# Kernel optimization log

Hardware: AMD Instinct MI355X
Metric: run time of the kernel (lower is better)

Reference implementation:

```python
import jax, jax.numpy as jnp
import numpy as np

NUM_HEADS = 16


def setup_inputs() -> dict:
    key = jax.random.key(0)
    k1, k2, k3 = jax.random.split(key, 3)
    B, S, E = 2, 2048, 1024
    hidden_states = jax.random.normal(k1, (B, S, E), dtype=jnp.float32)
    c_attn_w = jax.random.normal(k2, (E, 3 * E), dtype=jnp.float32) * 0.02
    c_attn_b = jnp.zeros((3 * E,), dtype=jnp.float32)
    c_proj_w = jax.random.normal(k3, (E, E), dtype=jnp.float32) * 0.02
    c_proj_b = jnp.zeros((E,), dtype=jnp.float32)
    return {
        "hidden_states": hidden_states,
        "c_attn_w": c_attn_w,
        "c_attn_b": c_attn_b,
        "c_proj_w": c_proj_w,
        "c_proj_b": c_proj_b,
    }


def reference(hidden_states, c_attn_w, c_attn_b, c_proj_w, c_proj_b):
    B, S, E = hidden_states.shape
    H = NUM_HEADS
    D = E // H
    # Conv1D: qkv projection -> [B, S, 3E]
    qkv = jnp.einsum("bse,ef->bsf", hidden_states, c_attn_w) + c_attn_b
    q, k, v = jnp.split(qkv, 3, axis=-1)
    # split heads -> [B, H, S, D]
    def heads(x):
        return x.reshape(B, S, H, D).transpose(0, 2, 1, 3)
    q, k, v = heads(q), heads(k), heads(v)
    # scaled QK^T -> [B, H, S, S]
    scale = jnp.asarray(D, dtype=q.dtype) ** 0.5
    attn_weights = jnp.einsum("bhqd,bhkd->bhqk", q, k) / scale
    # causal mask (bias buffer): True on/below diagonal
    causal = jnp.tril(jnp.ones((S, S), dtype=bool))
    mask_value = jnp.finfo(attn_weights.dtype).min
    attn_weights = jnp.where(causal[None, None, :, :], attn_weights, mask_value)
    attn_weights = jax.nn.softmax(attn_weights, axis=-1)
    # attn @ V -> merge heads -> [B, S, E]
    attn_out = jnp.einsum("bhqk,bhkd->bhqd", attn_weights, v)
    attn_out = attn_out.transpose(0, 2, 1, 3).reshape(B, S, E)
    # output projection (Conv1D)
    out = jnp.einsum("bse,ef->bsf", attn_out, c_proj_w) + c_proj_b
    return out
```

## Files before the change

kernel.cpp:

```cpp
#include <hip/hip_runtime.h>
#include <stdint.h>

typedef __attribute__((ext_vector_type(8))) __bf16 bf16x8;
typedef __attribute__((ext_vector_type(4))) __bf16 bf16x4;
typedef __attribute__((ext_vector_type(4))) float f32x4;

#define MFMA16(a, b, c) __builtin_amdgcn_mfma_f32_16x16x32_bf16(a, b, c, 0, 0, 0)

__device__ __forceinline__ void async_ld16(const __bf16* g, __bf16* lds_base) {
    __builtin_amdgcn_global_load_lds(
        (const __attribute__((address_space(1))) void*)g,
        (__attribute__((address_space(3))) void*)lds_base, 16, 0, 0);
}

__global__ __launch_bounds__(256) void k_prep(
    const float* __restrict__ hs, const float* __restrict__ w1,
    const float* __restrict__ w2, __bf16* __restrict__ hsb,
    __bf16* __restrict__ w1t, __bf16* __restrict__ w2t) {
    __shared__ __bf16 tile[32][33];
    int bid = blockIdx.x, tid = threadIdx.x;
    if (bid < 4096) {
        int i = (bid * 256 + tid) * 4;
        float4 v = *(const float4*)(hs + i);
        bf16x4 o;
        o.x = (__bf16)v.x; o.y = (__bf16)v.y; o.z = (__bf16)v.z; o.w = (__bf16)v.w;
        *(bf16x4*)(hsb + i) = o;
        return;
    }
    const float* in; __bf16* out; int C, tb;
    if (bid < 7168) { in = w1; out = w1t; C = 3072; tb = bid - 4096; }
    else            { in = w2; out = w2t; C = 1024; tb = bid - 7168; }
    const int R = 1024;
    int ntc = C >> 5;
    int c0 = (tb % ntc) * 32, r0 = (tb / ntc) * 32;
    int tx = tid & 31, ty = tid >> 5;
#pragma unroll
    for (int i = 0; i < 4; i++)
        tile[ty + i * 8][tx] = (__bf16)in[(size_t)(r0 + ty + i * 8) * C + c0 + tx];
    __syncthreads();
#pragma unroll
    for (int i = 0; i < 4; i++)
        out[(size_t)(c0 + ty + i * 8) * R + r0 + tx] = tile[tx][ty + i * 8];
}

__global__ __launch_bounds__(256, 3) void k_gemm_qkv(
    const __bf16* __restrict__ A, const __bf16* __restrict__ Bt,
    const float* __restrict__ bias,
    __bf16* __restrict__ Qo, __bf16* __restrict__ Ko, __bf16* __restrict__ Vo) {
    __shared__ __bf16 As[128 * 32];
    __shared__ __bf16 Bs[128 * 32];
    const int Kd = 1024;
    int lid = blockIdx.x;
    int xcd = lid & 7, c = lid >> 3;
    int mi = (xcd >> 1) * 8 + c / 12;
    int ni = (xcd & 1) * 12 + c % 12;
    int n0 = ni * 128, m0 = mi * 128;
    bool tr = (ni < 16);
    int tid = threadIdx.x;
    int wv = tid >> 6, lane = tid & 63;
    int wm = (wv >> 1) * 64, wn = (wv & 1) * 64;
    int quad = lane >> 4, l16 = lane & 15;
    int lrow = lane >> 2, lcol = (lane & 3) * 8;
    const __bf16* p0 = tr ? Bs : As;
    const __bf16* p1 = tr ? As : Bs;
    int o0 = tr ? wn : wm, o1 = tr ? wm : wn;
    f32x4 acc[4][4] = {};
    for (int k0 = 0; k0 < Kd; k0 += 32) {
        __syncthreads();
#pragma unroll
        for (int r = 0; r < 2; r++) {
            int row = r * 64 + wv * 16;
            async_ld16(&A[(size_t)(m0 + row + lrow) * Kd + k0 + lcol], &As[row * 32]);
            async_ld16(&Bt[(size_t)(n0 + row + lrow) * Kd + k0 + lcol], &Bs[row * 32]);
        }
        __syncthreads();
        bf16x8 f0[4], f1[4];
#pragma unroll
        for (int i = 0; i < 4; i++)
            f0[i] = *(const bf16x8*)(&p0[(o0 + i * 16 + l16) * 32 + quad * 8]);
#pragma unroll
        for (int j = 0; j < 4; j++)
            f1[j] = *(const bf16x8*)(&p1[(o1 + j * 16 + l16) * 32 + quad * 8]);
#pragma unroll
        for (int i = 0; i < 4; i++)
#pragma unroll
            for (int j = 0; j < 4; j++)
                acc[i][j] = MFMA16(f0[i], f1[j], acc[i][j]);
    }
    if (tr) {
#pragma unroll
        for (int i = 0; i < 4; i++) {
#pragma unroll
            for (int j = 0; j < 4; j++) {
                int nb = n0 + wn + i * 16 + quad * 4;
                int sec = nb >> 10, nl = nb & 1023;
                int h = nl >> 6, d = nl & 63;
                int sg = m0 + wm + j * 16 + l16;
                int bb = sg >> 11, s = sg & 2047;
                f32x4 bv = *(const f32x4*)(&bias[nb]);
                __bf16* dst = (sec == 0) ? Qo : Ko;
                float scl = (sec == 0) ? 0.1803368801f : 1.0f;
                bf16x4 q4;
#pragma unroll
                for (int r = 0; r < 4; r++)
                    q4[r] = (__bf16)((acc[i][j][r] + bv[r]) * scl);
                *(bf16x4*)(&dst[((size_t)(bb * 16 + h) * 2048 + s) * 64 + d]) = q4;
            }
        }
    } else {
#pragma unroll
        for (int i = 0; i < 4; i++) {
#pragma unroll
            for (int j = 0; j < 4; j++) {
                int n = n0 + wn + j * 16 + l16;
                float bv = bias[n];
                int nl = n & 1023;
                int h = nl >> 6, d = nl & 63;
                int mbase = m0 + wm + i * 16 + quad * 4;
                int bb = mbase >> 11, s = mbase & 2047;
                bf16x4 v4;
#pragma unroll
                for (int r = 0; r < 4; r++) v4[r] = (__bf16)(acc[i][j][r] + bv);
                *(bf16x4*)(&Vo[((size_t)(bb * 16 + h) * 64 + d) * 2048 + s]) = v4;
            }
        }
    }
}

__global__ __launch_bounds__(256, 3) void k_gemm_proj(
    const __bf16* __restrict__ A, const __bf16* __restrict__ Bt,
    const float* __restrict__ bias, float* __restrict__ out) {
    __shared__ __bf16 As[64 * 32];
    __shared__ __bf16 Bs[128 * 32];
    const int Kd = 1024;
    int lid = blockIdx.x;
    int xcd = lid & 7, c = lid >> 3;
    int mi = xcd * 8 + (c >> 3);
    int ni = c & 7;
    int n0 = ni * 128, m0 = mi * 64;
    int tid = threadIdx.x;
    int wv = tid >> 6, lane = tid & 63;
    int wm = (wv >> 1) * 32, wn = (wv & 1) * 64;
    int quad = lane >> 4, l16 = lane & 15;
    int lrow = lane >> 2, lcol = (lane & 3) * 8;
    f32x4 acc[4][2] = {};
    for (int k0 = 0; k0 < Kd; k0 += 32) {
        __syncthreads();
        async_ld16(&A[(size_t)(m0 + wv * 16 + lrow) * Kd + k0 + lcol], &As[(wv * 16) * 32]);
#pragma unroll
        for (int r = 0; r < 2; r++) {
            int row = r * 64 + wv * 16;
            async_ld16(&Bt[(size_t)(n0 + row + lrow) * Kd + k0 + lcol], &Bs[row * 32]);
        }
        __syncthreads();
        bf16x8 f0[4], f1[2];
#pragma unroll
        for (int i = 0; i < 4; i++)
            f0[i] = *(const bf16x8*)(&Bs[(wn + i * 16 + l16) * 32 + quad * 8]);
#pragma unroll
        for (int j = 0; j < 2; j++)
            f1[j] = *(const bf16x8*)(&As[(wm + j * 16 + l16) * 32 + quad * 8]);
#pragma unroll
        for (int i = 0; i < 4; i++)
#pragma unroll
            for (int j = 0; j < 2; j++)
                acc[i][j] = MFMA16(f0[i], f1[j], acc[i][j]);
    }
#pragma unroll
    for (int i = 0; i < 4; i++) {
#pragma unroll
        for (int j = 0; j < 2; j++) {
            int nb = n0 + wn + i * 16 + quad * 4;
            int m = m0 + wm + j * 16 + l16;
            f32x4 bv = *(const f32x4*)(&bias[nb]);
            f32x4 o = acc[i][j] + bv;
            *(f32x4*)(&out[(size_t)m * 1024 + nb]) = o;
        }
    }
}

__device__ const int ATT_ORDER[24] = {7, 8, 10, 12, 14, 16, 18, 20, 22, 23, 6, 21,
                                      5, 19, 4, 17, 3, 15, 2, 13, 1, 11, 0, 9};

__global__ __launch_bounds__(256, 3) void k_attn(
    const __bf16* __restrict__ Qg, const __bf16* __restrict__ Kg,
    const __bf16* __restrict__ Vtg, __bf16* __restrict__ Op, float* __restrict__ Lp) {
    __shared__ __bf16 Ksb[2][64 * 64];
    __shared__ __bf16 Vtb[2][64 * 64];
    __shared__ __bf16 Ps[128 * 72];
    int bh = blockIdx.x & 31;
    int slot = ATT_ORDER[blockIdx.x >> 5];
    int t, k0, k1;
    if (slot < 8) { t = slot; k0 = 0; k1 = 2 * t + 2; }
    else { int i2 = slot - 8; t = 8 + (i2 >> 1); k0 = (i2 & 1) * 16; k1 = min(k0 + 16, 2 * t + 2); }
    const __bf16* Qp = Qg + (size_t)bh * 2048 * 64;
    const __bf16* Kp = Kg + (size_t)bh * 2048 * 64;
    const __bf16* Vp = Vtg + (size_t)bh * 64 * 2048;
    int tid = threadIdx.x, wv = tid >> 6, lane = tid & 63;
    int quad = lane >> 4, l16 = lane & 15;
    int rl = lane >> 3, sj = lane & 7;
    int sgo = (sj ^ rl) << 3;
    int swl = l16 & 7;

    bf16x8 qf[2][2];
#pragma unroll
    for (int qn = 0; qn < 2; qn++)
#pragma unroll
        for (int ks = 0; ks < 2; ks++)
            qf[qn][ks] = *(const bf16x8*)(
                &Qp[(size_t)(t * 128 + wv * 32 + qn * 16 + l16) * 64 + ks * 32 + quad * 8]);
    const f32x4 zf = {0.f, 0.f, 0.f, 0.f};
    f32x4 lacc[2] = {zf, zf};
    f32x4 acc_o[2][4] = {};

    auto stage = [&](int buf, int kt) {
#pragma unroll
        for (int half = 0; half < 2; half++) {
            int r0 = wv * 16 + half * 8;
            async_ld16(&Kp[(size_t)(kt * 64 + r0 + rl) * 64 + sgo], &Ksb[buf][r0 * 64]);
            async_ld16(&Vp[(size_t)(r0 + rl) * 2048 + kt * 64 + sgo], &Vtb[buf][r0 * 64]);
        }
    };

    stage(0, k0);
    __syncthreads();

    for (int kt = k0; kt < k1; kt++) {
        int cur = (kt - k0) & 1;
        if (kt + 1 < k1) stage(cur ^ 1, kt + 1);
        const __bf16* Kc = Ksb[cur];
        const __bf16* Vc = Vtb[cur];
        f32x4 s[2][4];
#pragma unroll
        for (int ks = 0; ks < 2; ks++) {
            bf16x8 kf[4];
#pragma unroll
            for (int i = 0; i < 4; i++)
                kf[i] = *(const bf16x8*)(
                    &Kc[(i * 16 + l16) * 64 + (((ks * 4 + quad) ^ swl) << 3)]);
            __builtin_amdgcn_s_setprio(1);
#pragma unroll
            for (int i = 0; i < 4; i++)
#pragma unroll
                for (int qn = 0; qn < 2; qn++)
                    s[qn][i] = MFMA16(kf[i], qf[qn][ks], ks == 0 ? zf : s[qn][i]);
            __builtin_amdgcn_s_setprio(0);
        }
#pragma unroll
        for (int qn = 0; qn < 2; qn++) {
            int qmin = t * 128 + wv * 32 + qn * 16;
            if (kt * 64 + 63 > qmin) {
#pragma unroll
                for (int i = 0; i < 4; i++)
#pragma unroll
                    for (int r = 0; r < 4; r++)
                        if (kt * 64 + i * 16 + quad * 4 + r > qmin + l16) s[qn][i][r] = -1e30f;
            }
        }
#pragma unroll
        for (int qn = 0; qn < 2; qn++)
#pragma unroll
            for (int i = 0; i < 4; i++) {
                f32x4 pe;
#pragma unroll
                for (int r = 0; r < 4; r++) pe[r] = exp2f(s[qn][i][r]);
                lacc[qn] += pe;
                bf16x4 pk;
#pragma unroll
                for (int r = 0; r < 4; r++) pk[r] = (__bf16)pe[r];
                *(bf16x4*)(&Ps[(wv * 32 + qn * 16 + l16) * 72 + i * 16 + quad * 4]) = pk;
            }
#pragma unroll
        for (int ks = 0; ks < 2; ks++) {
            bf16x8 pf[2];
#pragma unroll
            for (int qn = 0; qn < 2; qn++)
                pf[qn] = *(const bf16x8*)(
                    &Ps[(wv * 32 + qn * 16 + l16) * 72 + ks * 32 + quad * 8]);
            bf16x8 vf[4];
#pragma unroll
            for (int i = 0; i < 4; i++)
                vf[i] = *(const bf16x8*)(
                    &Vc[(i * 16 + l16) * 64 + (((ks * 4 + quad) ^ swl) << 3)]);
            __builtin_amdgcn_s_setprio(1);
#pragma unroll
            for (int i = 0; i < 4; i++)
#pragma unroll
                for (int qn = 0; qn < 2; qn++)
                    acc_o[qn][i] = MFMA16(vf[i], pf[qn], acc_o[qn][i]);
            __builtin_amdgcn_s_setprio(0);
        }
        __syncthreads();
    }
    size_t pbase = (size_t)slot * 32 + bh;
#pragma unroll
    for (int qn = 0; qn < 2; qn++) {
        float ls = lacc[qn][0] + lacc[qn][1] + lacc[qn][2] + lacc[qn][3];
        ls += __shfl_xor(ls, 16);
        ls += __shfl_xor(ls, 32);
        int ql = wv * 32 + qn * 16 + l16;
        if (quad == 0) Lp[pbase * 128 + ql] = ls;
#pragma unroll
        for (int i = 0; i < 4; i++) {
            bf16x4 o4;
#pragma unroll
            for (int r = 0; r < 4; r++) o4[r] = (__bf16)acc_o[qn][i][r];
            *(bf16x4*)(&Op[(pbase * 128 + ql) * 64 + i * 16 + quad * 4]) = o4;
        }
    }
}

__global__ __launch_bounds__(256) void k_attn_combine(
    const __bf16* __restrict__ Op, const float* __restrict__ Lp,
    __bf16* __restrict__ AOb) {
    int gid = blockIdx.x * 256 + threadIdx.x;
    int d4 = gid & 15;
    int q = (gid >> 4) & 2047;
    int bh = gid >> 15;
    int t = q >> 7, ql = q & 127;
    int n = (t <= 7) ? 1 : 2;
    int base = (t <= 7) ? t : 8 + 2 * (t - 8);
    float L = 0.f, o[4] = {};
    for (int c = 0; c < n; c++) {
        size_t idx = (size_t)(base + c) * 32 + bh;
        L += Lp[idx * 128 + ql];
        bf16x4 p4 = *(const bf16x4*)(&Op[(idx * 128 + ql) * 64 + d4 * 4]);
#pragma unroll
        for (int r = 0; r < 4; r++) o[r] += (float)p4[r];
    }
    float inv = 1.f / L;
    int b = bh >> 4, h = bh & 15;
    bf16x4 o4;
#pragma unroll
    for (int r = 0; r < 4; r++) o4[r] = (__bf16)(o[r] * inv);
    *(bf16x4*)(&AOb[((size_t)b * 2048 + q) * 1024 + h * 64 + d4 * 4]) = o4;
}

extern "C" void kernel_launch(void* const* d_in, const int* in_sizes, int n_in,
                              void* d_out, int out_size, void* d_ws, size_t ws_size,
                              hipStream_t stream) {
    const float* hs = (const float*)d_in[0];
    const float* w1 = (const float*)d_in[1];
    const float* b1 = (const float*)d_in[2];
    const float* w2 = (const float*)d_in[3];
    const float* b2 = (const float*)d_in[4];
    float* out = (float*)d_out;

    char* ws = (char*)d_ws;
    __bf16* hsb = (__bf16*)(ws);
    __bf16* w1t = (__bf16*)(ws + (size_t)8 * 1024 * 1024);
    __bf16* w2t = (__bf16*)(ws + (size_t)14 * 1024 * 1024);
    __bf16* Qb  = (__bf16*)(ws + (size_t)16 * 1024 * 1024);
    __bf16* Kb  = (__bf16*)(ws + (size_t)24 * 1024 * 1024);
    __bf16* Vb  = (__bf16*)(ws + (size_t)32 * 1024 * 1024);
    __bf16* AOb = (__bf16*)(ws + (size_t)40 * 1024 * 1024);
    __bf16* Opart = (__bf16*)(ws);
    float*  Lpart = (float*)(ws + (size_t)13 * 1024 * 1024);

    k_prep<<<8192, 256, 0, stream>>>(hs, w1, w2, hsb, w1t, w2t);
    k_gemm_qkv<<<768, 256, 0, stream>>>(hsb, w1t, b1, Qb, Kb, Vb);
    k_attn<<<768, 256, 0, stream>>>(Qb, Kb, Vb, Opart, Lpart);
    k_attn_combine<<<4096, 256, 0, stream>>>(Opart, Lpart, AOb);
    k_gemm_proj<<<512, 256, 0, stream>>>(AOb, w2t, b2, out);
}
```

Before: 183.2 us.

## Double GEMM K-tile to 64 with swizzled LDS, skip masked attention tiles, reorder blocks

Both GEMM kernels now stage 64-wide K slices with an XOR-swizzled LDS layout, which halves the number of barrier pairs per K loop and is meant to cut LDS bank conflicts. The attention kernel lets each wave skip the compute for key tiles that lie entirely above its causal rows, while still taking part in staging and barriers. The attention block launch order table is also reshuffled to rebalance the work. The larger LDS footprint in the GEMMs may lower occupancy.

```diff
diff --git a/kernel.cpp b/kernel.cpp
--- a/kernel.cpp
+++ b/kernel.cpp
@@ -47,8 +47,8 @@
     const __bf16* __restrict__ A, const __bf16* __restrict__ Bt,
     const float* __restrict__ bias,
     __bf16* __restrict__ Qo, __bf16* __restrict__ Ko, __bf16* __restrict__ Vo) {
-    __shared__ __bf16 As[128 * 32];
-    __shared__ __bf16 Bs[128 * 32];
+    __shared__ __bf16 As[128 * 64];
+    __shared__ __bf16 Bs[128 * 64];
     const int Kd = 1024;
     int lid = blockIdx.x;
     int xcd = lid & 7, c = lid >> 3;
@@ -60,32 +60,39 @@
     int wv = tid >> 6, lane = tid & 63;
     int wm = (wv >> 1) * 64, wn = (wv & 1) * 64;
     int quad = lane >> 4, l16 = lane & 15;
-    int lrow = lane >> 2, lcol = (lane & 3) * 8;
+    int rl = lane >> 3, sj = lane & 7;
+    int sgo = (sj ^ rl) << 3;
+    int swl = l16 & 7;
     const __bf16* p0 = tr ? Bs : As;
     const __bf16* p1 = tr ? As : Bs;
     int o0 = tr ? wn : wm, o1 = tr ? wm : wn;
     f32x4 acc[4][4] = {};
-    for (int k0 = 0; k0 < Kd; k0 += 32) {
-        __syncthreads();
-#pragma unroll
-        for (int r = 0; r < 2; r++) {
-            int row = r * 64 + wv * 16;
-            async_ld16(&A[(size_t)(m0 + row + lrow) * Kd + k0 + lcol], &As[row * 32]);
-            async_ld16(&Bt[(size_t)(n0 + row + lrow) * Kd + k0 + lcol], &Bs[row * 32]);
-        }
-        __syncthreads();
-        bf16x8 f0[4], f1[4];
-#pragma unroll
-        for (int i = 0; i < 4; i++)
-            f0[i] = *(const bf16x8*)(&p0[(o0 + i * 16 + l16) * 32 + quad * 8]);
-#pragma unroll
-        for (int j = 0; j < 4; j++)
-            f1[j] = *(const bf16x8*)(&p1[(o1 + j * 16 + l16) * 32 + quad * 8]);
-#pragma unroll
-        for (int i = 0; i < 4; i++)
+    for (int k0 = 0; k0 < Kd; k0 += 64) {
+        __syncthreads();
+#pragma unroll
+        for (int r = 0; r < 4; r++) {
+            int row = wv * 32 + r * 8;
+            async_ld16(&A[(size_t)(m0 + row + rl) * Kd + k0 + sgo], &As[row * 64]);
+            async_ld16(&Bt[(size_t)(n0 + row + rl) * Kd + k0 + sgo], &Bs[row * 64]);
+        }
+        __syncthreads();
+#pragma unroll
+        for (int ks = 0; ks < 2; ks++) {
+            bf16x8 f0[4], f1[4];
+#pragma unroll
+            for (int i = 0; i < 4; i++)
+                f0[i] = *(const bf16x8*)(
+                    &p0[(o0 + i * 16 + l16) * 64 + (((ks * 4 + quad) ^ swl) << 3)]);
 #pragma unroll
             for (int j = 0; j < 4; j++)
-                acc[i][j] = MFMA16(f0[i], f1[j], acc[i][j]);
+                f1[j] = *(const bf16x8*)(
+                    &p1[(o1 + j * 16 + l16) * 64 + (((ks * 4 + quad) ^ swl) << 3)]);
+#pragma unroll
+            for (int i = 0; i < 4; i++)
+#pragma unroll
+                for (int j = 0; j < 4; j++)
+                    acc[i][j] = MFMA16(f0[i], f1[j], acc[i][j]);
+        }
     }
     if (tr) {
 #pragma unroll
@@ -130,8 +137,8 @@
 __global__ __launch_bounds__(256, 3) void k_gemm_proj(
     const __bf16* __restrict__ A, const __bf16* __restrict__ Bt,
     const float* __restrict__ bias, float* __restrict__ out) {
-    __shared__ __bf16 As[64 * 32];
-    __shared__ __bf16 Bs[128 * 32];
+    __shared__ __bf16 As[64 * 64];
+    __shared__ __bf16 Bs[128 * 64];
     const int Kd = 1024;
     int lid = blockIdx.x;
     int xcd = lid & 7, c = lid >> 3;
@@ -142,29 +149,40 @@
     int wv = tid >> 6, lane = tid & 63;
     int wm = (wv >> 1) * 32, wn = (wv & 1) * 64;
     int quad = lane >> 4, l16 = lane & 15;
-    int lrow = lane >> 2, lcol = (lane & 3) * 8;
+    int rl = lane >> 3, sj = lane & 7;
+    int sgo = (sj ^ rl) << 3;
+    int swl = l16 & 7;
     f32x4 acc[4][2] = {};
-    for (int k0 = 0; k0 < Kd; k0 += 32) {
-        __syncthreads();
-        async_ld16(&A[(size_t)(m0 + wv * 16 + lrow) * Kd + k0 + lcol], &As[(wv * 16) * 32]);
+    for (int k0 = 0; k0 < Kd; k0 += 64) {
+        __syncthreads();
 #pragma unroll
         for (int r = 0; r < 2; r++) {
-            int row = r * 64 + wv * 16;
-            async_ld16(&Bt[(size_t)(n0 + row + lrow) * Kd + k0 + lcol], &Bs[row * 32]);
-        }
-        __syncthreads();
-        bf16x8 f0[4], f1[2];
-#pragma unroll
-        for (int i = 0; i < 4; i++)
-            f0[i] = *(const bf16x8*)(&Bs[(wn + i * 16 + l16) * 32 + quad * 8]);
-#pragma unroll
-        for (int j = 0; j < 2; j++)
-            f1[j] = *(const bf16x8*)(&As[(wm + j * 16 + l16) * 32 + quad * 8]);
-#pragma unroll
-        for (int i = 0; i < 4; i++)
+            int row = wv * 16 + r * 8;
+            async_ld16(&A[(size_t)(m0 + row + rl) * Kd + k0 + sgo], &As[row * 64]);
+        }
+#pragma unroll
+        for (int r = 0; r < 4; r++) {
+            int row = wv * 32 + r * 8;
+            async_ld16(&Bt[(size_t)(n0 + row + rl) * Kd + k0 + sgo], &Bs[row * 64]);
+        }
+        __syncthreads();
+#pragma unroll
+        for (int ks = 0; ks < 2; ks++) {
+            bf16x8 f0[4], f1[2];
+#pragma unroll
+            for (int i = 0; i < 4; i++)
+                f0[i] = *(const bf16x8*)(
+                    &Bs[(wn + i * 16 + l16) * 64 + (((ks * 4 + quad) ^ swl) << 3)]);
 #pragma unroll
             for (int j = 0; j < 2; j++)
-                acc[i][j] = MFMA16(f0[i], f1[j], acc[i][j]);
+                f1[j] = *(const bf16x8*)(
+                    &As[(wm + j * 16 + l16) * 64 + (((ks * 4 + quad) ^ swl) << 3)]);
+#pragma unroll
+            for (int i = 0; i < 4; i++)
+#pragma unroll
+                for (int j = 0; j < 2; j++)
+                    acc[i][j] = MFMA16(f0[i], f1[j], acc[i][j]);
+        }
     }
 #pragma unroll
     for (int i = 0; i < 4; i++) {
@@ -179,8 +197,9 @@
     }
 }
 
-__device__ const int ATT_ORDER[24] = {7, 8, 10, 12, 14, 16, 18, 20, 22, 23, 6, 21,
-                                      5, 19, 4, 17, 3, 15, 2, 13, 1, 11, 0, 9};
+__device__ const int ATT_ORDER[24] = {7, 10, 14, 16, 18, 20, 22, 23,
+                                      8, 12, 6, 21, 5, 19, 4, 17,
+                                      0, 9, 1, 11, 2, 13, 3, 15};
 
 __global__ __launch_bounds__(256, 3) void k_attn(
     const __bf16* __restrict__ Qg, const __bf16* __restrict__ Kg,
@@ -212,6 +231,7 @@
     const f32x4 zf = {0.f, 0.f, 0.f, 0.f};
     f32x4 lacc[2] = {zf, zf};
     f32x4 acc_o[2][4] = {};
+    int qwmax = t * 128 + wv * 32 + 31;
 
     auto stage = [&](int buf, int kt) {
 #pragma unroll
@@ -228,67 +248,69 @@
     for (int kt = k0; kt < k1; kt++) {
         int cur = (kt - k0) & 1;
         if (kt + 1 < k1) stage(cur ^ 1, kt + 1);
-        const __bf16* Kc = Ksb[cur];
-        const __bf16* Vc = Vtb[cur];
-        f32x4 s[2][4];
-#pragma unroll
-        for (int ks = 0; ks < 2; ks++) {
-            bf16x8 kf[4];
-#pragma unroll
-            for (int i = 0; i < 4; i++)
-                kf[i] = *(const bf16x8*)(
-                    &Kc[(i * 16 + l16) * 64 + (((ks * 4 + quad) ^ swl) << 3)]);
-            __builtin_amdgcn_s_setprio(1);
-#pragma unroll
-            for (int i = 0; i < 4; i++)
+        if (kt * 64 <= qwmax) {
+            const __bf16* Kc = Ksb[cur];
+            const __bf16* Vc = Vtb[cur];
+            f32x4 s[2][4];
+#pragma unroll
+            for (int ks = 0; ks < 2; ks++) {
+                bf16x8 kf[4];
+#pragma unroll
+                for (int i = 0; i < 4; i++)
+                    kf[i] = *(const bf16x8*)(
+                        &Kc[(i * 16 + l16) * 64 + (((ks * 4 + quad) ^ swl) << 3)]);
+                __builtin_amdgcn_s_setprio(1);
+#pragma unroll
+                for (int i = 0; i < 4; i++)
+#pragma unroll
+                    for (int qn = 0; qn < 2; qn++)
+                        s[qn][i] = MFMA16(kf[i], qf[qn][ks], ks == 0 ? zf : s[qn][i]);
+                __builtin_amdgcn_s_setprio(0);
+            }
+#pragma unroll
+            for (int qn = 0; qn < 2; qn++) {
+                int qmin = t * 128 + wv * 32 + qn * 16;
+                if (kt * 64 + 63 > qmin) {
+#pragma unroll
+                    for (int i = 0; i < 4; i++)
+#pragma unroll
+                        for (int r = 0; r < 4; r++)
+                            if (kt * 64 + i * 16 + quad * 4 + r > qmin + l16) s[qn][i][r] = -1e30f;
+                }
+            }
+#pragma unroll
+            for (int qn = 0; qn < 2; qn++)
+#pragma unroll
+                for (int i = 0; i < 4; i++) {
+                    f32x4 pe;
+#pragma unroll
+                    for (int r = 0; r < 4; r++) pe[r] = exp2f(s[qn][i][r]);
+                    lacc[qn] += pe;
+                    bf16x4 pk;
+#pragma unroll
+                    for (int r = 0; r < 4; r++) pk[r] = (__bf16)pe[r];
+                    *(bf16x4*)(&Ps[(wv * 32 + qn * 16 + l16) * 72 + i * 16 + quad * 4]) = pk;
+                }
+#pragma unroll
+            for (int ks = 0; ks < 2; ks++) {
+                bf16x8 pf[2];
 #pragma unroll
                 for (int qn = 0; qn < 2; qn++)
-                    s[qn][i] = MFMA16(kf[i], qf[qn][ks], ks == 0 ? zf : s[qn][i]);
-            __builtin_amdgcn_s_setprio(0);
-        }
-#pragma unroll
-        for (int qn = 0; qn < 2; qn++) {
-            int qmin = t * 128 + wv * 32 + qn * 16;
-            if (kt * 64 + 63 > qmin) {
+                    pf[qn] = *(const bf16x8*)(
+                        &Ps[(wv * 32 + qn * 16 + l16) * 72 + ks * 32 + quad * 8]);
+                bf16x8 vf[4];
 #pragma unroll
                 for (int i = 0; i < 4; i++)
-#pragma unroll
-                    for (int r = 0; r < 4; r++)
-                        if (kt * 64 + i * 16 + quad * 4 + r > qmin + l16) s[qn][i][r] = -1e30f;
-            }
-        }
-#pragma unroll
-        for (int qn = 0; qn < 2; qn++)
-#pragma unroll
-            for (int i = 0; i < 4; i++) {
-                f32x4 pe;
-#pragma unroll
-                for (int r = 0; r < 4; r++) pe[r] = exp2f(s[qn][i][r]);
-                lacc[qn] += pe;
-                bf16x4 pk;
-#pragma unroll
-                for (int r = 0; r < 4; r++) pk[r] = (__bf16)pe[r];
-                *(bf16x4*)(&Ps[(wv * 32 + qn * 16 + l16) * 72 + i * 16 + quad * 4]) = pk;
-            }
-#pragma unroll
-        for (int ks = 0; ks < 2; ks++) {
-            bf16x8 pf[2];
-#pragma unroll
-            for (int qn = 0; qn < 2; qn++)
-                pf[qn] = *(const bf16x8*)(
-                    &Ps[(wv * 32 + qn * 16 + l16) * 72 + ks * 32 + quad * 8]);
-            bf16x8 vf[4];
-#pragma unroll
-            for (int i = 0; i < 4; i++)
-                vf[i] = *(const bf16x8*)(
-                    &Vc[(i * 16 + l16) * 64 + (((ks * 4 + quad) ^ swl) << 3)]);
-            __builtin_amdgcn_s_setprio(1);
-#pragma unroll
-            for (int i = 0; i < 4; i++)
-#pragma unroll
-                for (int qn = 0; qn < 2; qn++)
-                    acc_o[qn][i] = MFMA16(vf[i], pf[qn], acc_o[qn][i]);
-            __builtin_amdgcn_s_setprio(0);
+                    vf[i] = *(const bf16x8*)(
+                        &Vc[(i * 16 + l16) * 64 + (((ks * 4 + quad) ^ swl) << 3)]);
+                __builtin_amdgcn_s_setprio(1);
+#pragma unroll
+                for (int i = 0; i < 4; i++)
+#pragma unroll
+                    for (int qn = 0; qn < 2; qn++)
+                        acc_o[qn][i] = MFMA16(vf[i], pf[qn], acc_o[qn][i]);
+                __builtin_amdgcn_s_setprio(0);
+            }
         }
         __syncthreads();
     }
```

Measured after the change: 176.5 us. 1.04x faster.
